# Optimization experiments

Hardware: AMD Instinct MI355X
Metric: run time of the kernel (lower is better)

The kernel has to match this reference:

```python
import jax, jax.numpy as jnp
import numpy as np

T, H, E, I, K = 4096, 1024, 8, 1024, 2  # tokens, hidden, experts, intermediate, top_k


def setup_inputs() -> dict:
    key = jax.random.key(0)
    k1, k2, k3, k4, k5 = jax.random.split(key, 5)
    x = jax.random.normal(k1, (T, H), dtype=jnp.float32)
    router_logits = jax.random.normal(k2, (T, E), dtype=jnp.float32)
    per_expert_scale = jnp.ones((E,), dtype=jnp.float32)
    # FusedMoE layout: w13 = fused [gate; up] projection [E, 2I, H], w2 = down [E, H, I]
    w13 = jax.random.normal(k3, (E, 2 * I, H), dtype=jnp.float32) * 0.02
    w2 = jax.random.normal(k4, (E, H, I), dtype=jnp.float32) * 0.02
    return {"x": x, "router_logits": router_logits,
            "per_expert_scale": per_expert_scale, "w13": w13, "w2": w2}


def reference(x, router_logits, per_expert_scale, w13, w2):
    # --- Gemma4 routing: softmax over ALL experts -> top-k -> renormalize ---
    _, topk_ids = jax.lax.top_k(router_logits, K)              # [T, K] int32
    probs = jax.nn.softmax(router_logits, axis=-1)             # [T, E]
    indicator = jax.nn.one_hot(topk_ids, E, dtype=probs.dtype).sum(axis=-2)  # [T, E]
    gate = indicator * probs
    renorm = gate.sum(axis=-1, keepdims=True)
    renorm = jnp.where(renorm > 0.0, renorm, 1.0)
    dispatch = gate / renorm                                   # zero off top-k
    # per_expert_scale folded into routing weights (only top-k slots nonzero)
    combine_w = dispatch * per_expert_scale[None, :]           # [T, E]

    # --- expert FFN (gelu gate * up -> down), combined with routing weights ---
    w1, w3 = w13[:, :I, :], w13[:, I:, :]                      # [E, I, H] each
    g = jnp.einsum('th,eih->tei', x, w1)                       # gate proj
    u = jnp.einsum('th,eih->tei', x, w3)                       # up proj
    h = jax.nn.gelu(g, approximate=False) * u                  # exact GELU (torch default)
    y = jnp.einsum('tei,ehi->teh', h, w2)                      # down proj
    out = jnp.einsum('te,teh->th', combine_w, y)               # weighted combine
    return out
```

## Files before the change

kernel.cpp:

```cpp
#include <hip/hip_runtime.h>
#include <hip/hip_bf16.h>

#define T_TOK 4096
#define H_DIM 1024
#define E_NUM 8
#define I_DIM 1024
#define PAD_CAP 9216
#define RBLK 16
#define G1_ROWBLK (PAD_CAP / 128)

typedef __attribute__((ext_vector_type(4))) float f32x4;
typedef __attribute__((ext_vector_type(8))) short bf16x8;

__device__ __forceinline__ unsigned short f2b(float f) {
  union { float f; unsigned int u; } v; v.f = f;
  unsigned int r = v.u + 0x7fffu + ((v.u >> 16) & 1u);
  return (unsigned short)(r >> 16);
}

__device__ __forceinline__ void async_copy16(const void* g, void* l) {
  __builtin_amdgcn_global_load_lds(
      (const __attribute__((address_space(1))) void*)g,
      (__attribute__((address_space(3))) void*)l, 16, 0, 0);
}

__device__ __forceinline__ void conv_chunk(const float* __restrict__ src,
                                           unsigned short* __restrict__ dst,
                                           size_t base) {
  size_t i = base + (size_t)threadIdx.x * 8;
  float4 f0 = *(const float4*)(src + i);
  float4 f1 = *(const float4*)(src + i + 4);
  uint4 pk;
  pk.x = (unsigned)f2b(f0.x) | ((unsigned)f2b(f0.y) << 16);
  pk.y = (unsigned)f2b(f0.z) | ((unsigned)f2b(f0.w) << 16);
  pk.z = (unsigned)f2b(f1.x) | ((unsigned)f2b(f1.y) << 16);
  pk.w = (unsigned)f2b(f1.z) | ((unsigned)f2b(f1.w) << 16);
  *(uint4*)(dst + i) = pk;
}

__global__ __launch_bounds__(256) void k_prep(
    const float* __restrict__ x, const float* __restrict__ logits,
    const float* __restrict__ scale, const float* __restrict__ w13,
    unsigned short* __restrict__ xb, unsigned short* __restrict__ w13b,
    int* __restrict__ tids, float* __restrict__ cw, int* __restrict__ cnt) {
  const int b = blockIdx.x;
  if (b < RBLK) {
    __shared__ int s_cnt[E_NUM];
    const int tid = threadIdx.x;
    if (tid < E_NUM) s_cnt[tid] = 0;
    __syncthreads();
    int t = b * 256 + tid;
    float l[E_NUM];
    *(float4*)(l)     = *(const float4*)(logits + (size_t)t * E_NUM);
    *(float4*)(l + 4) = *(const float4*)(logits + (size_t)t * E_NUM + 4);
    float m = l[0];
#pragma unroll
    for (int i = 1; i < E_NUM; ++i) m = fmaxf(m, l[i]);
    float p[E_NUM]; float s = 0.f;
#pragma unroll
    for (int i = 0; i < E_NUM; ++i) { p[i] = expf(l[i] - m); s += p[i]; }
    int i0 = 0; float b0 = l[0];
#pragma unroll
    for (int i = 1; i < E_NUM; ++i) if (l[i] > b0) { b0 = l[i]; i0 = i; }
    int i1 = -1; float b1 = -1e30f;
#pragma unroll
    for (int i = 0; i < E_NUM; ++i) if (i != i0 && l[i] > b1) { b1 = l[i]; i1 = i; }
    float g0 = p[i0] / s, g1 = p[i1] / s;
    float r = g0 + g1;
    cw[t * 2]     = g0 / r * scale[i0];
    cw[t * 2 + 1] = g1 / r * scale[i1];
    tids[t * 2] = i0; tids[t * 2 + 1] = i1;
    atomicAdd(&s_cnt[i0], 1);
    atomicAdd(&s_cnt[i1], 1);
    __syncthreads();
    if (tid < E_NUM) cnt[b * E_NUM + tid] = s_cnt[tid];
    return;
  }
  const int cb = b - RBLK;
  if (cb < 2048) conv_chunk(x,   xb,   (size_t)cb * 2048);
  else           conv_chunk(w13, w13b, (size_t)(cb - 2048) * 2048);
}

__global__ __launch_bounds__(256) void k_scatter(
    const int* __restrict__ tids, const int* __restrict__ cnt,
    int* __restrict__ pad_off, int* __restrict__ perm, int* __restrict__ inv) {
  __shared__ int s_cnt[RBLK * E_NUM];
  __shared__ int s_tot[E_NUM];
  __shared__ int s_off[E_NUM];
  __shared__ int s_base[E_NUM];
  __shared__ int l_cnt[E_NUM];
  const int b = blockIdx.x, tid = threadIdx.x;
  if (tid < RBLK * E_NUM) s_cnt[tid] = cnt[tid];
  if (tid < E_NUM) l_cnt[tid] = 0;
  __syncthreads();
  if (tid < E_NUM) {
    int tot = 0;
#pragma unroll
    for (int bb = 0; bb < RBLK; ++bb) tot += s_cnt[bb * E_NUM + tid];
    s_tot[tid] = tot;
  }
  __syncthreads();
  if (tid < E_NUM) {
    int off = 0;
    for (int e = 0; e < tid; ++e) off += (s_tot[e] + 127) & ~127;
    s_off[tid] = off;
    int myb = off;
    for (int bb = 0; bb < b; ++bb) myb += s_cnt[bb * E_NUM + tid];
    s_base[tid] = myb;
    if (b == 0) {
      pad_off[tid] = off;
      if (tid == E_NUM - 1) pad_off[E_NUM] = off + ((s_tot[tid] + 127) & ~127);
    }
  }
  __syncthreads();
  if (b < E_NUM) {
    int start = s_off[b] + s_tot[b];
    int end   = s_off[b] + ((s_tot[b] + 127) & ~127);
    for (int i = start + tid; i < end; i += 256) perm[i] = -1;
  }
  int t = b * 256 + tid;
  int i0 = tids[t * 2], i1 = tids[t * 2 + 1];
  int r0 = atomicAdd(&l_cnt[i0], 1);
  int s0 = s_base[i0] + r0;
  perm[s0] = t * 2; inv[t * 2] = s0;
  int r1 = atomicAdd(&l_cnt[i1], 1);
  int s1 = s_base[i1] + r1;
  perm[s1] = t * 2 + 1; inv[t * 2 + 1] = s1;
}

__global__ __launch_bounds__(256, 2) void k_gemm1(
    const unsigned short* __restrict__ xbf,
    const unsigned short* __restrict__ w13b,
    const int* __restrict__ perm, const int* __restrict__ pad_off,
    unsigned short* __restrict__ h_buf,
    const float* __restrict__ w2, unsigned short* __restrict__ w2b) {
  __shared__ __align__(16) unsigned short a_lds[128 * 64];
  __shared__ __align__(16) unsigned short b_lds[128 * 64];
  const int by = blockIdx.y;
  if (by >= G1_ROWBLK) {
    int cb = (by - G1_ROWBLK) * 16 + blockIdx.x;
    conv_chunk(w2, w2b, (size_t)cb * 2048);
    return;
  }
  const int vid = blockIdx.x + 16 * by;
  const int xcd = vid & 7, j = vid >> 3;
  const int rb  = xcd * 9 + (j >> 4);
  const int cbx = j & 15;
  const int tid = threadIdx.x;
  const int wave = tid >> 6, lane = tid & 63;
  const int row0 = rb * 128;
  if (row0 >= pad_off[E_NUM]) return;
  int e = 0;
#pragma unroll
  for (int i = 1; i < E_NUM; ++i) if (row0 >= pad_off[i]) e = i;
  const int iBase = cbx * 64;

  const int srcChunk = (lane & 7) ^ ((lane >> 3) & 7);

  const unsigned short* agbase[4];
#pragma unroll
  for (int jj = 0; jj < 4; ++jj) {
    int r = jj * 32 + wave * 8 + (lane >> 3);
    int p = perm[row0 + r];
    int tok = (p < 0) ? 0 : (p >> 1);
    agbase[jj] = xbf + (size_t)tok * H_DIM + srcChunk * 8;
  }
  const unsigned short* bgbase[4];
#pragma unroll
  for (int jj = 0; jj < 4; ++jj) {
    int brow = jj * 32 + wave * 8 + (lane >> 3);
    int seg = brow >> 5, half = seg & 1;
    int col = iBase + (seg >> 1) * 32 + (brow & 31);
    bgbase[jj] = w13b + ((size_t)e * 2 * I_DIM + half * I_DIM + col) * H_DIM + srcChunk * 8;
  }

  f32x4 acc[4][4];
#pragma unroll
  for (int mi = 0; mi < 4; ++mi)
#pragma unroll
    for (int ni = 0; ni < 4; ++ni) acc[mi][ni] = (f32x4)(0.f);

  const int wm = wave >> 1, wn = wave & 1;
  const int ml = lane & 15, quad = lane >> 4;

  for (int k0 = 0; k0 < H_DIM; k0 += 64) {
    __syncthreads();
#pragma unroll
    for (int jj = 0; jj < 4; ++jj)
      async_copy16(agbase[jj] + k0, a_lds + (jj * 256 + wave * 64) * 8);
#pragma unroll
    for (int jj = 0; jj < 4; ++jj)
      async_copy16(bgbase[jj] + k0, b_lds + (jj * 256 + wave * 64) * 8);
    __syncthreads();
#pragma unroll
    for (int ks = 0; ks < 2; ++ks) {
      const int ch = ((ks * 4 + quad) ^ (ml & 7)) * 8;
      bf16x8 af[4], bfr[4];
#pragma unroll
      for (int mi = 0; mi < 4; ++mi)
        af[mi] = *(const bf16x8*)(a_lds + (wm * 64 + mi * 16 + ml) * 64 + ch);
#pragma unroll
      for (int ni = 0; ni < 4; ++ni)
        bfr[ni] = *(const bf16x8*)(b_lds + (wn * 64 + ni * 16 + ml) * 64 + ch);
#pragma unroll
      for (int mi = 0; mi < 4; ++mi)
#pragma unroll
        for (int ni = 0; ni < 4; ++ni)
          acc[mi][ni] = __builtin_amdgcn_mfma_f32_16x16x32_bf16(af[mi], bfr[ni], acc[mi][ni], 0, 0, 0);
    }
  }
#pragma unroll
  for (int mi = 0; mi < 4; ++mi) {
#pragma unroll
    for (int nc = 0; nc < 2; ++nc) {
      f32x4 g = acc[mi][nc];
      f32x4 uu = acc[mi][nc + 2];
#pragma unroll
      for (int r = 0; r < 4; ++r) {
        int row = row0 + wm * 64 + mi * 16 + quad * 4 + r;
        int col = iBase + wn * 32 + nc * 16 + ml;
        float gg = g[r];
        float q  = gg * (2.3022080f + 0.10294324f * gg * gg);
        float z  = __builtin_amdgcn_exp2f(-q);
        float hv = gg * uu[r] * __builtin_amdgcn_rcpf(1.f + z);
        h_buf[(size_t)row * I_DIM + col] = f2b(hv);
      }
    }
  }
}

__global__ __launch_bounds__(256, 3) void k_gemm2(
    const unsigned short* __restrict__ h_buf,
    const unsigned short* __restrict__ w2b,
    const int* __restrict__ pad_off,
    unsigned short* __restrict__ y) {
  __shared__ __align__(16) unsigned short a_lds[128 * 64];
  __shared__ __align__(16) unsigned short b_lds[128 * 64];
  const int vid = blockIdx.x + 8 * blockIdx.y;
  const int xcd = vid & 7, j = vid >> 3;
  const int rb  = xcd * 9 + (j >> 3);
  const int cbx = j & 7;
  const int tid = threadIdx.x;
  const int wave = tid >> 6, lane = tid & 63;
  const int row0 = rb * 128;
  if (row0 >= pad_off[E_NUM]) return;
  int e = 0;
#pragma unroll
  for (int i = 1; i < E_NUM; ++i) if (row0 >= pad_off[i]) e = i;
  const int cBase = cbx * 128;
  const int srcChunk = (lane & 7) ^ ((lane >> 3) & 7);

  const unsigned short* agbase[4];
#pragma unroll
  for (int jj = 0; jj < 4; ++jj) {
    int r = jj * 32 + wave * 8 + (lane >> 3);
    agbase[jj] = h_buf + (size_t)(row0 + r) * I_DIM + srcChunk * 8;
  }
  const unsigned short* bgbase[4];
#pragma unroll
  for (int jj = 0; jj < 4; ++jj) {
    int brow = jj * 32 + wave * 8 + (lane >> 3);
    bgbase[jj] = w2b + ((size_t)e * H_DIM + cBase + brow) * I_DIM + srcChunk * 8;
  }
  f32x4 acc[4][4];
#pragma unroll
  for (int mi = 0; mi < 4; ++mi)
#pragma unroll
    for (int ni = 0; ni < 4; ++ni) acc[mi][ni] = (f32x4)(0.f);

  const int wm = wave >> 1, wn = wave & 1;
  const int ml = lane & 15, quad = lane >> 4;

  for (int k0 = 0; k0 < I_DIM; k0 += 64) {
    __syncthreads();
#pragma unroll
    for (int jj = 0; jj < 4; ++jj)
      async_copy16(agbase[jj] + k0, a_lds + (jj * 256 + wave * 64) * 8);
#pragma unroll
    for (int jj = 0; jj < 4; ++jj)
      async_copy16(bgbase[jj] + k0, b_lds + (jj * 256 + wave * 64) * 8);
    __syncthreads();
#pragma unroll
    for (int ks = 0; ks < 2; ++ks) {
      const int ch = ((ks * 4 + quad) ^ (ml & 7)) * 8;
      bf16x8 af[4], bfr[4];
#pragma unroll
      for (int mi = 0; mi < 4; ++mi)
        af[mi] = *(const bf16x8*)(a_lds + (wm * 64 + mi * 16 + ml) * 64 + ch);
#pragma unroll
      for (int ni = 0; ni < 4; ++ni)
        bfr[ni] = *(const bf16x8*)(b_lds + (wn * 64 + ni * 16 + ml) * 64 + ch);
#pragma unroll
      for (int mi = 0; mi < 4; ++mi)
#pragma unroll
        for (int ni = 0; ni < 4; ++ni)
          acc[mi][ni] = __builtin_amdgcn_mfma_f32_16x16x32_bf16(af[mi], bfr[ni], acc[mi][ni], 0, 0, 0);
    }
  }
#pragma unroll
  for (int mi = 0; mi < 4; ++mi) {
#pragma unroll
    for (int ni = 0; ni < 4; ++ni) {
#pragma unroll
      for (int r = 0; r < 4; ++r) {
        int row = row0 + wm * 64 + mi * 16 + quad * 4 + r;
        int col = cBase + wn * 64 + ni * 16 + ml;
        y[(size_t)row * H_DIM + col] = f2b(acc[mi][ni][r]);
      }
    }
  }
}

__global__ void k_combine(const unsigned short* __restrict__ y,
                          const int* __restrict__ inv, const float* __restrict__ cw,
                          float* __restrict__ out) {
  const int t = blockIdx.x;
  const int c = threadIdx.x * 4;
  int s0 = inv[t * 2], s1 = inv[t * 2 + 1];
  float c0 = cw[t * 2], c1 = cw[t * 2 + 1];
  uint2 a = *(const uint2*)(y + (size_t)s0 * H_DIM + c);
  uint2 b = *(const uint2*)(y + (size_t)s1 * H_DIM + c);
  union { unsigned v; float f; } w;
  float4 o;
  float alo, ahi, blo, bhi;
  w.v = a.x << 16;          alo = w.f;
  w.v = a.x & 0xffff0000u;  ahi = w.f;
  w.v = b.x << 16;          blo = w.f;
  w.v = b.x & 0xffff0000u;  bhi = w.f;
  o.x = c0 * alo + c1 * blo;
  o.y = c0 * ahi + c1 * bhi;
  w.v = a.y << 16;          alo = w.f;
  w.v = a.y & 0xffff0000u;  ahi = w.f;
  w.v = b.y << 16;          blo = w.f;
  w.v = b.y & 0xffff0000u;  bhi = w.f;
  o.z = c0 * alo + c1 * blo;
  o.w = c0 * ahi + c1 * bhi;
  *(float4*)(out + (size_t)t * H_DIM + c) = o;
}

extern "C" void kernel_launch(void* const* d_in, const int* in_sizes, int n_in,
                              void* d_out, int out_size, void* d_ws, size_t ws_size,
                              hipStream_t stream) {
  const float* x      = (const float*)d_in[0];
  const float* logits = (const float*)d_in[1];
  const float* scale  = (const float*)d_in[2];
  const float* w13    = (const float*)d_in[3];
  const float* w2     = (const float*)d_in[4];
  float* out = (float*)d_out;

  char* ws = (char*)d_ws;
  int*   pad_off = (int*)(ws + 128);
  int*   cnt     = (int*)(ws + 1024);
  int*   tids    = (int*)(ws + 4096);
  float* cw      = (float*)(ws + 65536);
  int*   perm    = (int*)(ws + 131072);
  int*   inv     = (int*)(ws + 196608);
  unsigned short* xb    = (unsigned short*)(ws + 0x40000);
  unsigned short* h_buf = (unsigned short*)(ws + 0x900000);
  unsigned short* w13b  = (unsigned short*)(ws + 0x1C00000);
  unsigned short* ybuf  = w13b;
  unsigned short* w2b   = (unsigned short*)(ws + 0x3C00000);

  k_prep<<<10240 + RBLK, 256, 0, stream>>>(x, logits, scale, w13,
                                           xb, w13b, tids, cw, cnt);
  k_scatter<<<RBLK, 256, 0, stream>>>(tids, cnt, pad_off, perm, inv);
  k_gemm1<<<dim3(16, G1_ROWBLK + 256), 256, 0, stream>>>(xb, w13b, perm, pad_off,
                                                         h_buf, w2, w2b);
  k_gemm2<<<dim3(8, PAD_CAP / 128), 256, 0, stream>>>(h_buf, w2b, pad_off, ybuf);
  k_combine<<<T_TOK, 256, 0, stream>>>(ybuf, inv, cw, out);
}
```

Baseline: 222.5 us.

## Fuse weighted combine into down-proj GEMM epilogue via atomic adds

Drops the separate combine kernel and the bf16 intermediate y buffer. The down-projection epilogue now looks up each row's token through perm, scales by its routing weight and atomically adds into the fp32 output. The output is zeroed by extra blocks in the prep kernel. This removes one launch plus the y write and read, but adds fp32 atomics (two contributions per output element) and makes the summation order nondeterministic.

```diff
diff --git a/kernel.cpp b/kernel.cpp
--- a/kernel.cpp
+++ b/kernel.cpp
@@ -42,7 +42,8 @@
     const float* __restrict__ x, const float* __restrict__ logits,
     const float* __restrict__ scale, const float* __restrict__ w13,
     unsigned short* __restrict__ xb, unsigned short* __restrict__ w13b,
-    int* __restrict__ tids, float* __restrict__ cw, int* __restrict__ cnt) {
+    int* __restrict__ tids, float* __restrict__ cw, int* __restrict__ cnt,
+    float* __restrict__ out) {
   const int b = blockIdx.x;
   if (b < RBLK) {
     __shared__ int s_cnt[E_NUM];
@@ -77,13 +78,19 @@
     return;
   }
   const int cb = b - RBLK;
-  if (cb < 2048) conv_chunk(x,   xb,   (size_t)cb * 2048);
-  else           conv_chunk(w13, w13b, (size_t)(cb - 2048) * 2048);
+  if (cb < 2048)        conv_chunk(x,   xb,   (size_t)cb * 2048);
+  else if (cb < 10240)  conv_chunk(w13, w13b, (size_t)(cb - 2048) * 2048);
+  else {
+    size_t i = (size_t)(cb - 10240) * 2048 + (size_t)threadIdx.x * 8;
+    uint4 z = {0u, 0u, 0u, 0u};
+    *(uint4*)(out + i)     = z;
+    *(uint4*)(out + i + 4) = z;
+  }
 }
 
 __global__ __launch_bounds__(256) void k_scatter(
     const int* __restrict__ tids, const int* __restrict__ cnt,
-    int* __restrict__ pad_off, int* __restrict__ perm, int* __restrict__ inv) {
+    int* __restrict__ pad_off, int* __restrict__ perm) {
   __shared__ int s_cnt[RBLK * E_NUM];
   __shared__ int s_tot[E_NUM];
   __shared__ int s_off[E_NUM];
@@ -121,11 +128,9 @@
   int t = b * 256 + tid;
   int i0 = tids[t * 2], i1 = tids[t * 2 + 1];
   int r0 = atomicAdd(&l_cnt[i0], 1);
-  int s0 = s_base[i0] + r0;
-  perm[s0] = t * 2; inv[t * 2] = s0;
+  perm[s_base[i0] + r0] = t * 2;
   int r1 = atomicAdd(&l_cnt[i1], 1);
-  int s1 = s_base[i1] + r1;
-  perm[s1] = t * 2 + 1; inv[t * 2 + 1] = s1;
+  perm[s_base[i1] + r1] = t * 2 + 1;
 }
 
 __global__ __launch_bounds__(256, 2) void k_gemm1(
@@ -232,8 +237,9 @@
 __global__ __launch_bounds__(256, 3) void k_gemm2(
     const unsigned short* __restrict__ h_buf,
     const unsigned short* __restrict__ w2b,
-    const int* __restrict__ pad_off,
-    unsigned short* __restrict__ y) {
+    const int* __restrict__ pad_off, const int* __restrict__ perm,
+    const float* __restrict__ cw,
+    float* __restrict__ out) {
   __shared__ __align__(16) unsigned short a_lds[128 * 64];
   __shared__ __align__(16) unsigned short b_lds[128 * 64];
   const int vid = blockIdx.x + 8 * blockIdx.y;
@@ -300,42 +306,19 @@
 #pragma unroll
   for (int mi = 0; mi < 4; ++mi) {
 #pragma unroll
-    for (int ni = 0; ni < 4; ++ni) {
-#pragma unroll
-      for (int r = 0; r < 4; ++r) {
-        int row = row0 + wm * 64 + mi * 16 + quad * 4 + r;
-        int col = cBase + wn * 64 + ni * 16 + ml;
-        y[(size_t)row * H_DIM + col] = f2b(acc[mi][ni][r]);
+    for (int r = 0; r < 4; ++r) {
+      int row = row0 + wm * 64 + mi * 16 + quad * 4 + r;
+      int p = perm[row];
+      if (p >= 0) {
+        float wgt = cw[p];
+        int tok = p >> 1;
+        float* o = out + (size_t)tok * H_DIM + cBase + wn * 64 + ml;
+#pragma unroll
+        for (int ni = 0; ni < 4; ++ni)
+          atomicAdd(o + ni * 16, wgt * acc[mi][ni][r]);
       }
     }
   }
-}
-
-__global__ void k_combine(const unsigned short* __restrict__ y,
-                          const int* __restrict__ inv, const float* __restrict__ cw,
-                          float* __restrict__ out) {
-  const int t = blockIdx.x;
-  const int c = threadIdx.x * 4;
-  int s0 = inv[t * 2], s1 = inv[t * 2 + 1];
-  float c0 = cw[t * 2], c1 = cw[t * 2 + 1];
-  uint2 a = *(const uint2*)(y + (size_t)s0 * H_DIM + c);
-  uint2 b = *(const uint2*)(y + (size_t)s1 * H_DIM + c);
-  union { unsigned v; float f; } w;
-  float4 o;
-  float alo, ahi, blo, bhi;
-  w.v = a.x << 16;          alo = w.f;
-  w.v = a.x & 0xffff0000u;  ahi = w.f;
-  w.v = b.x << 16;          blo = w.f;
-  w.v = b.x & 0xffff0000u;  bhi = w.f;
-  o.x = c0 * alo + c1 * blo;
-  o.y = c0 * ahi + c1 * bhi;
-  w.v = a.y << 16;          alo = w.f;
-  w.v = a.y & 0xffff0000u;  ahi = w.f;
-  w.v = b.y << 16;          blo = w.f;
-  w.v = b.y & 0xffff0000u;  bhi = w.f;
-  o.z = c0 * alo + c1 * blo;
-  o.w = c0 * ahi + c1 * bhi;
-  *(float4*)(out + (size_t)t * H_DIM + c) = o;
 }
 
 extern "C" void kernel_launch(void* const* d_in, const int* in_sizes, int n_in,
@@ -354,18 +337,16 @@
   int*   tids    = (int*)(ws + 4096);
   float* cw      = (float*)(ws + 65536);
   int*   perm    = (int*)(ws + 131072);
-  int*   inv     = (int*)(ws + 196608);
   unsigned short* xb    = (unsigned short*)(ws + 0x40000);
   unsigned short* h_buf = (unsigned short*)(ws + 0x900000);
   unsigned short* w13b  = (unsigned short*)(ws + 0x1C00000);
-  unsigned short* ybuf  = w13b;
   unsigned short* w2b   = (unsigned short*)(ws + 0x3C00000);
 
-  k_prep<<<10240 + RBLK, 256, 0, stream>>>(x, logits, scale, w13,
-                                           xb, w13b, tids, cw, cnt);
-  k_scatter<<<RBLK, 256, 0, stream>>>(tids, cnt, pad_off, perm, inv);
+  k_prep<<<12288 + RBLK, 256, 0, stream>>>(x, logits, scale, w13,
+                                           xb, w13b, tids, cw, cnt, out);
+  k_scatter<<<RBLK, 256, 0, stream>>>(tids, cnt, pad_off, perm);
   k_gemm1<<<dim3(16, G1_ROWBLK + 256), 256, 0, stream>>>(xb, w13b, perm, pad_off,
                                                          h_buf, w2, w2b);
-  k_gemm2<<<dim3(8, PAD_CAP / 128), 256, 0, stream>>>(h_buf, w2b, pad_off, ybuf);
-  k_combine<<<T_TOK, 256, 0, stream>>>(ybuf, inv, cw, out);
-}
+  k_gemm2<<<dim3(8, PAD_CAP / 128), 256, 0, stream>>>(h_buf, w2b, pad_off,
+                                                      perm, cw, out);
+}
```

Measured after the change: 235.4 us. +5.8%, slower.
